# Kernel tuning notes

Hardware: AMD Instinct MI355X
Metric: run time of the kernel (lower is better)

Reference implementation:

```python
import jax, jax.numpy as jnp
import numpy as np
from math import factorial

N_NODES = 20000
N_EDGES = 80000
NUM_GRAPHS = 64
NUM_NEIGHBORS = 3.8
POOL_NODES = 4.0  # num_nodes=4 constant in source forward

# ---------------- real Wigner 3j (e3nn-style, Frobenius norm 1) ----------------

def _w3j_complex(j1, j2, j3, m1, m2, m3):
    if m1 + m2 + m3 != 0:
        return 0.0
    t1 = j2 - m1 - j3; t2 = j1 + m2 - j3; t3 = j1 + j2 - j3
    t4 = j1 - m1; t5 = j2 + m2
    tmin = max(0, t1, t2); tmax = min(t3, t4, t5)
    if tmin > tmax:
        return 0.0
    s = 0.0
    for t in range(tmin, tmax + 1):
        s += (-1.0) ** t / (factorial(t) * factorial(t - t1) * factorial(t - t2)
                            * factorial(t3 - t) * factorial(t4 - t) * factorial(t5 - t))
    tri = (factorial(j1 + j2 - j3) * factorial(j1 - j2 + j3) * factorial(-j1 + j2 + j3)
           / factorial(j1 + j2 + j3 + 1))
    norm = np.sqrt(tri * factorial(j1 + m1) * factorial(j1 - m1) * factorial(j2 + m2)
                   * factorial(j2 - m2) * factorial(j3 + m3) * factorial(j3 - m3))
    return (-1.0) ** (j1 - j2 - m3) * norm * s


def _real_basis(l):
    U = np.zeros((2 * l + 1, 2 * l + 1), dtype=np.complex128)
    U[l, l] = 1.0
    for m in range(1, l + 1):
        U[l + m, l + m] = (-1) ** m / np.sqrt(2.0)
        U[l + m, l - m] = 1.0 / np.sqrt(2.0)
        U[l - m, l - m] = 1j / np.sqrt(2.0)
        U[l - m, l + m] = -1j * (-1) ** m / np.sqrt(2.0)
    return U

_W3J_CACHE = {}

def w3j(l1, l2, l3):
    key = (l1, l2, l3)
    if key not in _W3J_CACHE:
        C = np.zeros((2 * l1 + 1, 2 * l2 + 1, 2 * l3 + 1), dtype=np.complex128)
        for m1 in range(-l1, l1 + 1):
            for m2 in range(-l2, l2 + 1):
                m3 = -(m1 + m2)
                if -l3 <= m3 <= l3:
                    C[m1 + l1, m2 + l2, m3 + l3] = _w3j_complex(l1, l2, l3, m1, m2, m3)
        C = np.einsum('ia,jb,kc,abc->ijk', _real_basis(l1), _real_basis(l2), _real_basis(l3), C)
        C = np.real((-1j) ** (l1 + l2 + l3) * C)
        _W3J_CACHE[key] = jnp.asarray(C, dtype=jnp.float32)
    return _W3J_CACHE[key]

# ---------------- irreps bookkeeping ----------------
SH        = [(1, 0, 1), (1, 1, -1), (1, 2, 1), (1, 3, -1)]            # 1x0e+1x1o+1x2e+1x3o (dim 16)
GATE1_IN  = [(16,0,1),(16,0,-1),(8,0,1),(8,0,-1),(8,0,1),(8,0,-1),(16,1,-1),(16,1,1)]  # dim 160
GATE1_OUT = [(16,0,1),(16,0,1),(16,1,-1),(16,1,1)]                     # dim 128
GATE2_IN  = [(16,0,1),(16,0,-1),(6,0,1),(6,0,-1),(6,0,1),(6,0,-1),(12,1,-1),(12,1,1)]  # dim 128
GATE2_OUT = [(16,0,1),(16,0,1),(12,1,-1),(12,1,1)]                     # dim 104
OUT_FINAL = [(1, 0, 1)]


def slices(irreps):
    out = []; o = 0
    for m, l, p in irreps:
        d = m * (2 * l + 1); out.append((o, o + d)); o += d
    return out


def tp_paths(ir1, ir2, iro):
    paths = []
    for i1, (m1, l1, p1) in enumerate(ir1):
        for i2, (m2, l2, p2) in enumerate(ir2):
            for io, (mo, lo, po) in enumerate(iro):
                if po == p1 * p2 and abs(l1 - l2) <= lo <= l1 + l2:
                    paths.append((i1, i2, io))
    fan = [0] * len(iro)
    for i1, i2, io in paths:
        fan[io] += ir1[i1][0] * ir2[i2][0]
    numel = sum(ir1[i1][0] * ir2[i2][0] * iro[io][0] for i1, i2, io in paths)
    return paths, fan, numel


def tensor_product(x1, x2, weights, ir1, ir2, iro):
    # FullyConnectedTensorProduct, component norm, element path normalization
    paths, fan, numel = tp_paths(ir1, ir2, iro)
    s1, s2 = slices(ir1), slices(ir2)
    E = x1.shape[0]
    out_parts = [jnp.zeros((E, m * (2 * l + 1)), x1.dtype) for m, l, p in iro]
    wofs = 0
    for i1, i2, io in paths:
        m1, l1, _ = ir1[i1]; m2, l2, _ = ir2[i2]; mo, lo, _ = iro[io]
        n = m1 * m2 * mo
        w = weights[:, wofs:wofs + n].reshape(E, m1, m2, mo); wofs += n
        a = x1[:, s1[i1][0]:s1[i1][1]].reshape(E, m1, 2 * l1 + 1)
        b = x2[:, s2[i2][0]:s2[i2][1]].reshape(E, m2, 2 * l2 + 1)
        C = w3j(l1, l2, lo)
        pw = np.sqrt((2 * lo + 1) / fan[io])
        seg = jnp.einsum('eui,evj,ijk,euvw->ewk', a, b, C, w) * pw
        out_parts[io] = out_parts[io] + seg.reshape(E, mo * (2 * lo + 1))
    return jnp.concatenate(out_parts, axis=1)

# ---------------- activations / gate ----------------
_xs = np.linspace(-8.0, 8.0, 100001)
_pdf = np.exp(-0.5 * _xs ** 2) / np.sqrt(2 * np.pi)
TANH_NORM = float(1.0 / np.sqrt(np.sum(np.tanh(_xs) ** 2 * _pdf) * (_xs[1] - _xs[0])))
SQRT2 = float(np.sqrt(2.0))
ACT = {'relu': lambda t: jnp.maximum(t, 0.0) * SQRT2,
       'abs':  lambda t: jnp.abs(t),
       'tanh': lambda t: jnp.tanh(t) * TANH_NORM}


def gate_fn(x, scalars, gates, gated):
    o = 0; outs = []
    for m, a in scalars:
        outs.append(ACT[a](x[:, o:o + m])); o += m
    gv = []
    for m, a in gates:
        gv.append(ACT[a](x[:, o:o + m])); o += m
    g = jnp.concatenate(gv, axis=-1)
    gi = 0
    for m, l in gated:
        d = 2 * l + 1
        feat = x[:, o:o + m * d].reshape(-1, m, d)
        outs.append((feat * g[:, gi:gi + m, None]).reshape(-1, m * d))
        o += m * d; gi += m
    return jnp.concatenate(outs, axis=-1)

# ---------------- edge features ----------------

def sh_component(v):
    # real spherical harmonics l=0..3, 'component' normalization, unit input
    x, y, z = v[:, 0], v[:, 1], v[:, 2]
    s3, s5, s15 = np.sqrt(3.0), np.sqrt(5.0), np.sqrt(15.0)
    s7, s42, s70, s105 = np.sqrt(7.0), np.sqrt(42.0), np.sqrt(70.0), np.sqrt(105.0)
    Y0 = jnp.ones_like(x)[:, None]
    Y1 = jnp.stack([s3 * y, s3 * z, s3 * x], -1)
    Y2 = jnp.stack([s15 * x * y, s15 * y * z, 0.5 * s5 * (3 * z * z - 1.0),
                    s15 * x * z, 0.5 * s15 * (x * x - y * y)], -1)
    Y3 = jnp.stack([0.25 * s70 * y * (3 * x * x - y * y), s105 * x * y * z,
                    0.25 * s42 * y * (5 * z * z - 1.0), 0.5 * s7 * z * (5 * z * z - 3.0),
                    0.25 * s42 * x * (5 * z * z - 1.0), 0.5 * s105 * z * (x * x - y * y),
                    0.25 * s70 * x * (x * x - 3 * y * y)], -1)
    return jnp.concatenate([Y0, Y1, Y2, Y3], -1)  # [E,16]


def soft_one_hot(r):
    # soft_one_hot_linspace(start=0.5,end=2.5,number=3,basis='smooth_finite',cutoff=True)
    values = np.linspace(0.5, 2.5, 5)[1:-1]
    step = values[1] - values[0]
    diff = (r[:, None] - values) / step
    def f(u):
        return jnp.where(u > 0, jnp.exp(-1.0 / jnp.where(u > 0, u, 1.0)), 0.0)
    y = 1.14136 * np.exp(2.0) * f(diff + 1.0) * f(1.0 - diff)
    return y * np.sqrt(3.0)


def fc(x, w1, w2):
    # e3nn FullyConnectedNet([3,256,numel], relu)
    h = jnp.maximum(x @ (w1 / np.sqrt(w1.shape[0])), 0.0) * SQRT2
    return h @ (w2 / np.sqrt(w2.shape[0]))


def convolution(node_feats, edge_src, edge_dst, edge_attr, edge_scalars, w1, w2, ir_in, ir_out, n_nodes):
    weight = fc(edge_scalars, w1, w2)                                   # [E, numel]
    ef = tensor_product(node_feats[edge_src], edge_attr, weight, ir_in, SH, ir_out)
    return jax.ops.segment_sum(ef, edge_dst, num_segments=n_nodes) / np.sqrt(NUM_NEIGHBORS)


def _forward(pos, w1_1, w2_1, w1_2, w2_2, w1_3, w2_3, edge_src, edge_dst, batch):
    N = pos.shape[0]
    vec = pos[edge_src] - pos[edge_dst]
    r = jnp.sqrt(jnp.sum(vec * vec, axis=1) + 1e-12)
    unit = vec / r[:, None]
    edge_attr = sh_component(unit)
    edge_scalars = soft_one_hot(r)
    x = jax.ops.segment_sum(edge_attr, edge_dst, num_segments=N) / np.sqrt(NUM_NEIGHBORS)
    x = convolution(x, edge_src, edge_dst, edge_attr, edge_scalars, w1_1, w2_1, SH, GATE1_IN, N)
    x = gate_fn(x, [(16, 'relu'), (16, 'abs')], [(8, 'relu'), (8, 'tanh'), (8, 'relu'), (8, 'tanh')], [(16, 1), (16, 1)])
    x = convolution(x, edge_src, edge_dst, edge_attr, edge_scalars, w1_2, w2_2, GATE1_OUT, GATE2_IN, N)
    x = gate_fn(x, [(16, 'relu'), (16, 'abs')], [(6, 'relu'), (6, 'tanh'), (6, 'relu'), (6, 'tanh')], [(12, 1), (12, 1)])
    x = convolution(x, edge_src, edge_dst, edge_attr, edge_scalars, w1_3, w2_3, GATE2_OUT, OUT_FINAL, N)
    x = jax.ops.segment_sum(x, batch, num_segments=NUM_GRAPHS) / np.sqrt(POOL_NODES)
    return jax.nn.sigmoid(x)


def setup_inputs():
    key = jax.random.key(0)
    ks = jax.random.split(key, 10)
    pos = jax.random.normal(ks[0], (N_NODES, 3), jnp.float32) * 1.5
    edge_src = jax.random.randint(ks[1], (N_EDGES,), 0, N_NODES)
    edge_dst = jax.random.randint(ks[2], (N_EDGES,), 0, N_NODES)
    batch = jnp.sort(jax.random.randint(ks[3], (N_NODES,), 0, NUM_GRAPHS))
    _, _, n1 = tp_paths(SH, SH, GATE1_IN)
    _, _, n2 = tp_paths(GATE1_OUT, SH, GATE2_IN)
    _, _, n3 = tp_paths(GATE2_OUT, SH, OUT_FINAL)
    w1_1 = jax.random.normal(ks[4], (3, 256), jnp.float32)
    w2_1 = jax.random.normal(ks[5], (256, n1), jnp.float32)
    w1_2 = jax.random.normal(ks[6], (3, 256), jnp.float32)
    w2_2 = jax.random.normal(ks[7], (256, n2), jnp.float32)
    w1_3 = jax.random.normal(ks[8], (3, 256), jnp.float32)
    w2_3 = jax.random.normal(ks[9], (256, n3), jnp.float32)
    return {'pos': pos, 'w1_1': w1_1, 'w2_1': w2_1, 'w1_2': w1_2, 'w2_2': w2_2,
            'w1_3': w1_3, 'w2_3': w2_3, 'edge_src': edge_src, 'edge_dst': edge_dst, 'batch': batch}


def reference(pos, w1_1, w2_1, w1_2, w2_2, w1_3, w2_3, edge_src, edge_dst, batch):
    return _forward(pos, w1_1, w2_1, w1_2, w2_2, w1_3, w2_3, edge_src, edge_dst, batch)
```

## Files before the change

kernel.cpp:

```cpp
#include <hip/hip_runtime.h>
#include <math.h>

#define NNODE 20000
#define NEDGE 80000
#define NGRAPH 64

#define OFF_TANH  656
#define OFF_CNT   660
#define OFF_GSUM  664
#define OFF_HIST  7680
#define OFF_OFFS  9728
#define OFF_CUR   11784
#define OFF_EATTR 14336
#define OFF_RBUF  1294336
#define OFF_EINFO 1374336
#define OFF_X0    1694336
#define OFF_Y1    2014336
#define OFF_Y2    5214336
#define OFF_X1    7774336
#define OFF_X2    10334336
#define OFF_TAB   12414336

#define T000 0
#define T110 1
#define T220 10
#define T330 35
#define T011 84
#define T101 93
#define T111 102
#define T121 129
#define T211 174
#define T231 219
#define T321 324
#define T221 429
#define T331 504

#define INV_SQRT_NEIGH 0.5129891760425771f
#define SQRT2F 1.4142135623730951f

struct TabD { int l1,l2,l3,off; };
constexpr TabD HTABS[13] = {
  {0,0,0,T000},{1,1,0,T110},{2,2,0,T220},{3,3,0,T330},
  {0,1,1,T011},{1,0,1,T101},{1,1,1,T111},{1,2,1,T121},
  {2,1,1,T211},{2,3,1,T231},{3,2,1,T321},{2,2,1,T221},{3,3,1,T331}
};

struct CoreD { short a_off, b_off; short l1,l2,l3; short tab; short coff; short m1; };
struct PathD { short core; short wofs, wend, ooff; short mo, lo; float pw; };

constexpr CoreD HCORES1[13] = {
  {0,0, 0,0,0, T000, 0, 1},
  {0,1, 0,1,1, T011, 1, 1},
  {1,0, 1,0,1, T101, 4, 1},
  {1,1, 1,1,0, T110, 7, 1},
  {1,1, 1,1,1, T111, 8, 1},
  {1,4, 1,2,1, T121, 11, 1},
  {4,1, 2,1,1, T211, 14, 1},
  {4,4, 2,2,0, T220, 17, 1},
  {4,4, 2,2,1, T221, 18, 1},
  {4,9, 2,3,1, T231, 21, 1},
  {9,4, 3,2,1, T321, 24, 1},
  {9,9, 3,3,0, T330, 27, 1},
  {9,9, 3,3,1, T331, 28, 1}
};
#define PWR 0.7071067811865476f
constexpr PathD HPATHS1[21] = {
  {0,  0, 16,  0,16,0,0.5f},
  {0, 16, 24, 32, 8,0,0.5f},
  {0, 24, 32, 48, 8,0,0.5f},
  {1, 32, 48, 64,16,1,PWR},
  {2, 48, 64, 64,16,1,PWR},
  {3, 64, 80,  0,16,0,0.5f},
  {3, 80, 88, 32, 8,0,0.5f},
  {3, 88, 96, 48, 8,0,0.5f},
  {4, 96,112,112,16,1,1.0f},
  {5,112,128, 64,16,1,PWR},
  {6,128,144, 64,16,1,PWR},
  {7,144,160,  0,16,0,0.5f},
  {7,160,168, 32, 8,0,0.5f},
  {7,168,176, 48, 8,0,0.5f},
  {8,176,192,112,16,1,1.0f},
  {9,192,208, 64,16,1,PWR},
  {10,208,224,64,16,1,PWR},
  {11,224,240, 0,16,0,0.5f},
  {11,240,248,32, 8,0,0.5f},
  {11,248,256,48, 8,0,0.5f},
  {12,256,272,112,16,1,1.0f}
};

constexpr CoreD HCORES2[12] = {
  {0,0,  0,0,0, T000, 0,   16},
  {0,1,  0,1,1, T011, 16,  16},
  {16,0, 0,0,0, T000, 64,  16},
  {16,1, 0,1,1, T011, 80,  16},
  {32,0, 1,0,1, T101, 128, 16},
  {32,1, 1,1,0, T110, 176, 16},
  {32,1, 1,1,1, T111, 192, 16},
  {32,4, 1,2,1, T121, 240, 16},
  {80,0, 1,0,1, T101, 288, 16},
  {80,1, 1,1,0, T110, 336, 16},
  {80,1, 1,1,1, T111, 352, 16},
  {80,4, 1,2,1, T121, 400, 16}
};
#define PA 0.14433756729740643f
#define PB 0.25f
#define PC 0.19364916731037085f
constexpr PathD HPATHS2[20] = {
  {0,   0, 256,  0,16,0,PA},
  {0, 256, 352, 32, 6,0,PA},
  {0, 352, 448, 44, 6,0,PA},
  {1, 448, 640, 56,12,1,PC},
  {2, 640, 896,  0,16,0,PA},
  {2, 896, 992, 32, 6,0,PA},
  {2, 992,1088, 44, 6,0,PA},
  {3,1088,1280, 56,12,1,PC},
  {4,1280,1472, 56,12,1,PC},
  {5,1472,1728,  0,16,0,PA},
  {5,1728,1824, 32, 6,0,PA},
  {5,1824,1920, 44, 6,0,PA},
  {6,1920,2112, 92,12,1,PB},
  {7,2112,2304, 56,12,1,PC},
  {8,2304,2496, 92,12,1,PB},
  {9,2496,2752, 16,16,0,PB},
  {9,2752,2848, 38, 6,0,PB},
  {9,2848,2944, 50, 6,0,PB},
  {10,2944,3136,56,12,1,PC},
  {11,3136,3328,92,12,1,PB}
};

constexpr CoreD HCORES3[3] = {
  {0,0,  0,0,0, T000, 0,  16},
  {16,0, 0,0,0, T000, 16, 16},
  {32,1, 1,1,0, T110, 32, 12}
};
#define PD 0.15075567228888181f
constexpr PathD HPATHS3[3] = {
  {0, 0,16, 0,1,0,PD},
  {1,16,32, 0,1,0,PD},
  {2,32,44, 0,1,0,PD}
};

constexpr double FACT[9] = {1.0,1.0,2.0,6.0,24.0,120.0,720.0,5040.0,40320.0};

constexpr double csqrt_(double x){
  if(x<=0.0) return 0.0;
  double g = (x<1.0)? 1.0 : x;
  for(int i=0;i<40;i++) g = 0.5*(g + x/g);
  return g;
}

constexpr double cw3j_(int j1,int j2,int j3,int m1,int m2,int m3){
  if(m1+m2+m3!=0) return 0.0;
  int t1=j2-m1-j3, t2=j1+m2-j3, t3=j1+j2-j3, t4=j1-m1, t5=j2+m2;
  int tmin=t1>0?t1:0; if(t2>tmin) tmin=t2;
  int tmax=t3<t4?t3:t4; if(t5<tmax) tmax=t5;
  if(tmin>tmax) return 0.0;
  double s=0.0;
  for(int t=tmin;t<=tmax;++t){
    double d=FACT[t]*FACT[t-t1]*FACT[t-t2]*FACT[t3-t]*FACT[t4-t]*FACT[t5-t];
    s += ((t&1)? -1.0:1.0)/d;
  }
  double tri=FACT[j1+j2-j3]*FACT[j1-j2+j3]*FACT[-j1+j2+j3]/FACT[j1+j2+j3+1];
  double nrm=csqrt_(tri*FACT[j1+m1]*FACT[j1-m1]*FACT[j2+m2]*FACT[j2-m2]*FACT[j3+m3]*FACT[j3-m3]);
  return (((j1-j2-m3)&1)? -1.0:1.0)*nrm*s;
}

constexpr int curow_(int l,int i,int* a,double* re,double* im){
  const double is2=0.7071067811865475;
  int m=i-l;
  if(m==0){ a[0]=l; re[0]=1.0; im[0]=0.0; return 1; }
  if(m>0){
    a[0]=l+m; re[0]=((m&1)? -is2:is2); im[0]=0.0;
    a[1]=l-m; re[1]=is2; im[1]=0.0; return 2;
  }
  int mm=-m;
  a[0]=l-mm; re[0]=0.0; im[0]=is2;
  a[1]=l+mm; re[1]=0.0; im[1]=((mm&1)? is2:-is2);
  return 2;
}

constexpr float cw3j_elem_(int l1,int l2,int l3,int i,int j,int k){
  int aa[2]={0,0},bb[2]={0,0},cc[2]={0,0};
  double ar[2]={0,0},ai[2]={0,0},br[2]={0,0},bi[2]={0,0},cr[2]={0,0},ci[2]={0,0};
  int na=curow_(l1,i,aa,ar,ai);
  int nb=curow_(l2,j,bb,br,bi);
  int nc=curow_(l3,k,cc,cr,ci);
  double accr=0.0, acci=0.0;
  for(int x=0;x<na;x++)for(int y=0;y<nb;y++)for(int w=0;w<nc;w++){
    double wv=cw3j_(l1,l2,l3, aa[x]-l1, bb[y]-l2, cc[w]-l3);
    if(wv==0.0) continue;
    double pr=ar[x]*br[y]-ai[x]*bi[y];
    double pi=ar[x]*bi[y]+ai[x]*br[y];
    double qr=pr*cr[w]-pi*ci[w];
    double qi=pr*ci[w]+pi*cr[w];
    accr+=qr*wv; acci+=qi*wv;
  }
  int Lm=(l1+l2+l3)&3;
  double res = (Lm==0)? accr : (Lm==1)? acci : (Lm==2)? -accr : -acci;
  return (float)res;
}

struct WApart { float v[429]; };
constexpr WApart gen_wa_(){
  WApart o{};
  for(int t=0;t<11;t++){
    int l1=HTABS[t].l1,l2=HTABS[t].l2,l3=HTABS[t].l3;
    int n2=2*l2+1,n3=2*l3+1;
    int tot=(2*l1+1)*n2*n3;
    for(int z=0;z<tot;z++){
      int i=z/(n2*n3), j=(z/n3)%n2, k=z%n3;
      o.v[HTABS[t].off+z]=cw3j_elem_(l1,l2,l3,i,j,k);
    }
  }
  return o;
}
struct WBpart { float v[222]; };
constexpr WBpart gen_wb_(){
  WBpart o{};
  for(int t=11;t<13;t++){
    int l1=HTABS[t].l1,l2=HTABS[t].l2,l3=HTABS[t].l3;
    int n2=2*l2+1,n3=2*l3+1;
    int tot=(2*l1+1)*n2*n3;
    for(int z=0;z<tot;z++){
      int i=z/(n2*n3), j=(z/n3)%n2, k=z%n3;
      o.v[HTABS[t].off-429+z]=cw3j_elem_(l1,l2,l3,i,j,k);
    }
  }
  return o;
}
constexpr WApart WAC = gen_wa_();
constexpr WBpart WBC = gen_wb_();
struct W3Full { float v[651]; };
constexpr W3Full gen_wfull_(){
  W3Full f{};
  for(int i=0;i<429;i++) f.v[i]=WAC.v[i];
  for(int i=0;i<222;i++) f.v[429+i]=WBC.v[i];
  return f;
}
__constant__ W3Full W3JC = gen_wfull_();

template<int NW> struct PwArr { float v[NW]; };
template<int NW,int NP>
constexpr PwArr<NW> gen_pw_(const PathD (&P)[NP]){
  PwArr<NW> a{};
  for(int p=0;p<NP;p++)
    for(int j=P[p].wofs;j<P[p].wend;j++) a.v[j]=P[p].pw;
  return a;
}
__constant__ PwArr<272>  PWC1 = gen_pw_<272>(HPATHS1);
__constant__ PwArr<3328> PWC2 = gen_pw_<3328>(HPATHS2);
__constant__ PwArr<44>   PWC3 = gen_pw_<44>(HPATHS3);

struct OutSeg { int mult, l; };
constexpr OutSeg OSEG1[8] = {{16,0},{16,0},{8,0},{8,0},{8,0},{8,0},{16,1},{16,1}};
constexpr OutSeg OSEG2[8] = {{16,0},{16,0},{6,0},{6,0},{6,0},{6,0},{12,1},{12,1}};
constexpr OutSeg OSEG3[1] = {{1,0}};

struct Ent2 { int jb, cb, nu; };
template<int NCOL,int NENT,int NW> struct ColMetaT {
  int cidx[NCOL+1];
  int obase[NCOL];
  int n3c[NCOL];
  Ent2 ent[NENT];
  int newj[NW];
};

template<int NCOL,int NENT,int NW,int NSEG,int NP,int NC>
constexpr ColMetaT<NCOL,NENT,NW> gen_colmeta_(const OutSeg (&S)[NSEG], const PathD (&P)[NP], const CoreD (&C)[NC]){
  ColMetaT<NCOL,NENT,NW> m{};
  int col=0, cnt=0, o=0, nb=0;
  for(int s=0;s<NSEG;s++){
    int n3=2*S[s].l+1;
    for(int wc=0;wc<S[s].mult;wc++){
      m.cidx[col]=cnt;
      int ob=o+wc*n3;
      m.obase[col]=ob;
      m.n3c[col]=n3;
      for(int p=0;p<NP;p++){
        PathD pd=P[p];
        int pn3=2*pd.lo+1;
        if(pn3!=n3) continue;
        int rel=ob-pd.ooff;
        if(rel<0||rel>=pd.mo*pn3) continue;
        int w=rel/pn3;
        CoreD cd=C[pd.core];
        int m1=cd.m1;
        m.ent[cnt]=Ent2{nb,(int)cd.coff,m1};
        for(int u=0;u<m1;u++) m.newj[pd.wofs + w + u*pd.mo]=nb+u;
        nb+=m1;
        cnt++;
      }
      col++;
    }
    o+=S[s].mult*n3;
  }
  m.cidx[col]=cnt;
  return m;
}

__constant__ ColMetaT<96,272,272>  CMETA1 = gen_colmeta_<96,272,272>(OSEG1, HPATHS1, HCORES1);
__constant__ ColMetaT<80,208,3328> CMETA2 = gen_colmeta_<80,208,3328>(OSEG2, HPATHS2, HCORES2);
__constant__ ColMetaT< 1,  3,  44> CMETA3 = gen_colmeta_< 1,  3,  44>(OSEG3, HPATHS3, HCORES3);

struct CItem { short aoff, boff, n1, n2, cofs, jstep, woff, pad; };
struct CArr1 { CItem it[31]; };
constexpr CArr1 gen_c1_(){
  CArr1 a{}; int s=0;
  for(int cn=0;cn<13;cn++){
    CoreD cd=HCORES1[cn];
    int n1=2*cd.l1+1,n2=2*cd.l2+1,n3=2*cd.l3+1;
    for(int k=0;k<n3;k++){
      a.it[s]=CItem{cd.a_off,cd.b_off,(short)n1,(short)n2,(short)(cd.tab+k),(short)n3,(short)(cd.coff+k),0};
      s++;
    }
  }
  return a;
}
__constant__ CArr1 CIT1 = gen_c1_();

struct Fam { short b_off, tab, n1, n2, n3, goff; };
constexpr Fam GF2[6]={
  {0,T000,1,1,1,0},{1,T011,1,3,3,1},{0,T101,3,1,3,4},
  {1,T110,3,3,1,13},{1,T111,3,3,3,16},{4,T121,3,5,3,25}};
constexpr Fam GF3[2]={{0,T000,1,1,1,0},{1,T110,3,3,1,1}};
struct CoreG { short fam,a_off,m1,coff; };
constexpr CoreG CG2[12]={
  {0,0,16,0},{1,0,16,16},{0,16,16,64},{1,16,16,80},
  {2,32,16,128},{3,32,16,176},{4,32,16,192},{5,32,16,240},
  {2,80,16,288},{3,80,16,336},{4,80,16,352},{5,80,16,400}};
constexpr CoreG CG3[3]={{0,0,16,0},{0,16,16,16},{1,32,12,32}};

struct GItem { short boff, cofs, n2, jstep; };
template<int NG> struct GArrT { GItem it[NG]; };
template<int NG,int NF>
constexpr GArrT<NG> gen_g_(const Fam (&F)[NF]){
  GArrT<NG> a{}; int s=0;
  for(int f=0;f<NF;f++){
    for(int i=0;i<F[f].n1;i++)for(int k=0;k<F[f].n3;k++){
      a.it[s]=GItem{F[f].b_off,(short)(F[f].tab + i*F[f].n2*F[f].n3 + k),F[f].n2,F[f].n3};
      s++;
    }
  }
  return a;
}
__constant__ GArrT<34> GIT2=gen_g_<34>(GF2);
__constant__ GArrT<4>  GIT3=gen_g_<4>(GF3);

struct OItem { short aoff, gofs, n1, n3, woff, pad; };
template<int NO> struct OArrT { OItem it[NO]; };
template<int NO,int NC,int NF>
constexpr OArrT<NO> gen_o_(const CoreG (&C)[NC], const Fam (&F)[NF]){
  OArrT<NO> a{}; int s=0;
  for(int cn=0;cn<NC;cn++){
    Fam f=F[C[cn].fam];
    for(int k=0;k<f.n3;k++)for(int u=0;u<C[cn].m1;u++){
      a.it[s]=OItem{(short)(C[cn].a_off+u*f.n1),(short)(f.goff+k),f.n1,f.n3,
                    (short)(C[cn].coff+k*C[cn].m1+u),0};
      s++;
    }
  }
  return a;
}
__constant__ OArrT<448> OIT2=gen_o_<448,12,6>(CG2,GF2);
__constant__ OArrT<44>  OIT3=gen_o_<44,3,2>(CG3,GF3);

template<int CNT,int N3,int NCOLS>
__device__ __forceinline__ void apply1_col(const Ent2* __restrict__ ep, const float* __restrict__ T0,
    const float* __restrict__ crb, float fr, float&a0,float&a1,float&a2){
  const float* tja=T0+ep[0].jb;
  float wv[CNT];
  #pragma unroll
  for(int t=0;t<CNT;t++){
    float w0=tja[t], w1=tja[t+NCOLS];
    wv[t]=w0+fr*(w1-w0);
  }
  #pragma unroll
  for(int t=0;t<CNT;t++){
    const float* cr=crb+ep[t].cb;
    a0=fmaf(wv[t],cr[0],a0);
    if constexpr(N3==3){ a1=fmaf(wv[t],cr[1],a1); a2=fmaf(wv[t],cr[2],a2); }
  }
}
__device__ __forceinline__ void apply1_dyn(const Ent2* __restrict__ ep, int cnt, int n3,
    const float* __restrict__ T0, const float* __restrict__ crb, float fr, int NCOLS,
    float&a0,float&a1,float&a2){
  const float* tja=T0+ep[0].jb;
  for(int t=0;t<cnt;t++){
    float w0=tja[t], w1=tja[t+NCOLS];
    float w=w0+fr*(w1-w0);
    const float* cr=crb+ep[t].cb;
    a0=fmaf(w,cr[0],a0);
    if(n3==3){ a1=fmaf(w,cr[1],a1); a2=fmaf(w,cr[2],a2); }
  }
}
template<int CNT,int N3,int NCOLS>
__device__ __forceinline__ void apply2_col(const Ent2* __restrict__ ep, const float* __restrict__ T0,
    const float* __restrict__ crb, float fr, float&a0,float&a1,float&a2){
  #pragma unroll
  for(int t=0;t<CNT;t++){
    const float* cr=crb+ep[t].cb;
    const float* tj=T0+ep[t].jb;
    #pragma unroll
    for(int uu=0;uu<16;uu+=4){
      float4 w0=*(const float4*)(tj+uu);
      float4 w1=*(const float4*)(tj+NCOLS+uu);
      float w;
      if constexpr(N3==1){
        float4 cv=*(const float4*)(cr+uu);
        w=w0.x+fr*(w1.x-w0.x); a0=fmaf(w,cv.x,a0);
        w=w0.y+fr*(w1.y-w0.y); a0=fmaf(w,cv.y,a0);
        w=w0.z+fr*(w1.z-w0.z); a0=fmaf(w,cv.z,a0);
        w=w0.w+fr*(w1.w-w0.w); a0=fmaf(w,cv.w,a0);
      } else {
        float4 c0=*(const float4*)(cr+uu);
        float4 c1=*(const float4*)(cr+16+uu);
        float4 c2=*(const float4*)(cr+32+uu);
        w=w0.x+fr*(w1.x-w0.x); a0=fmaf(w,c0.x,a0); a1=fmaf(w,c1.x,a1); a2=fmaf(w,c2.x,a2);
        w=w0.y+fr*(w1.y-w0.y); a0=fmaf(w,c0.y,a0); a1=fmaf(w,c1.y,a1); a2=fmaf(w,c2.y,a2);
        w=w0.z+fr*(w1.z-w0.z); a0=fmaf(w,c0.z,a0); a1=fmaf(w,c1.z,a1); a2=fmaf(w,c2.z,a2);
        w=w0.w+fr*(w1.w-w0.w); a0=fmaf(w,c0.w,a0); a1=fmaf(w,c1.w,a1); a2=fmaf(w,c2.w,a2);
      }
    }
  }
}
__device__ __forceinline__ void apply2_dyn(const Ent2* __restrict__ ep, int cnt, int n3,
    const float* __restrict__ T0, const float* __restrict__ crb, float fr, int NCOLS,
    float&a0,float&a1,float&a2){
  for(int t=0;t<cnt;t++){
    const float* cr=crb+ep[t].cb;
    const float* tj=T0+ep[t].jb;
    #pragma unroll
    for(int uu=0;uu<16;uu+=4){
      float4 w0=*(const float4*)(tj+uu);
      float4 w1=*(const float4*)(tj+NCOLS+uu);
      float w;
      if(n3==1){
        float4 cv=*(const float4*)(cr+uu);
        w=w0.x+fr*(w1.x-w0.x); a0=fmaf(w,cv.x,a0);
        w=w0.y+fr*(w1.y-w0.y); a0=fmaf(w,cv.y,a0);
        w=w0.z+fr*(w1.z-w0.z); a0=fmaf(w,cv.z,a0);
        w=w0.w+fr*(w1.w-w0.w); a0=fmaf(w,cv.w,a0);
      } else {
        float4 c0=*(const float4*)(cr+uu);
        float4 c1=*(const float4*)(cr+16+uu);
        float4 c2=*(const float4*)(cr+32+uu);
        w=w0.x+fr*(w1.x-w0.x); a0=fmaf(w,c0.x,a0); a1=fmaf(w,c1.x,a1); a2=fmaf(w,c2.x,a2);
        w=w0.y+fr*(w1.y-w0.y); a0=fmaf(w,c0.y,a0); a1=fmaf(w,c1.y,a1); a2=fmaf(w,c2.y,a2);
        w=w0.z+fr*(w1.z-w0.z); a0=fmaf(w,c0.z,a0); a1=fmaf(w,c1.z,a1); a2=fmaf(w,c2.z,a2);
        w=w0.w+fr*(w1.w-w0.w); a0=fmaf(w,c0.w,a0); a1=fmaf(w,c1.w,a1); a2=fmaf(w,c2.w,a2);
      }
    }
  }
}

__global__ __launch_bounds__(256) void k_tables(
    const float* __restrict__ W1_1, const float* __restrict__ W2_1, float* __restrict__ T1,
    const float* __restrict__ W1_2, const float* __restrict__ W2_2, float* __restrict__ T2,
    const float* __restrict__ W1_3, const float* __restrict__ W2_3, float* __restrict__ T3,
    int R, int NR, float* __restrict__ ws){
  int tid=threadIdx.x;
  int by=blockIdx.y;
  if(by==16){
    if(blockIdx.x!=0) return;
    for(int i=tid;i<(728-OFF_CNT);i+=256) ws[OFF_CNT+i]=0.0f;
    for(int i=tid;i<(13832-OFF_HIST);i+=256) ws[OFF_HIST+i]=0.0f;
    __shared__ double red[256];
    double loc=0.0;
    for(int i=tid;i<=100000;i+=256){
      float x=-8.0f+16.0f*(float)i/100000.0f;
      float th=tanhf(x);
      float pdf=expf(-0.5f*x*x)*0.3989422804014327f;
      loc += (double)(th*th*pdf);
    }
    red[tid]=loc; __syncthreads();
    for(int s=128;s>0;s>>=1){ if(tid<s) red[tid]+=red[tid+s]; __syncthreads(); }
    if(tid==0) ws[OFF_TANH]=(float)(1.0/sqrt(red[0]*(16.0/100000.0)));
    return;
  }
  int conv, ybase;
  const float* W1; const float* W2; float* tab; int NCOLS; float scale;
  if(by<2){ conv=1; ybase=by;   W1=W1_1; W2=W2_1; tab=T1; NCOLS=272;  scale=INV_SQRT_NEIGH; }
  else if(by<15){ conv=2; ybase=by-2; W1=W1_2; W2=W2_2; tab=T2; NCOLS=3328; scale=INV_SQRT_NEIGH; }
  else { conv=3; ybase=0;  W1=W1_3; W2=W2_3; tab=T3; NCOLS=44;   scale=INV_SQRT_NEIGH*0.5f; }

  __shared__ float sh_h[256][16];
  int r0=blockIdx.x*16;
  {
    int c=tid;
    float wa=W1[c], wb=W1[256+c], wc=W1[512+c];
    const float A=(float)(1.14136*7.38905609893065*1.7320508075688772);
    for(int k=0;k<16;k++){
      int ri=r0+k;
      float r=0.5f+2.0f*(float)ri/(float)NR;
      float sv[3];
      #pragma unroll
      for(int j=0;j<3;j++){
        float v=1.0f+0.5f*(float)j;
        float diff=(r-v)*2.0f;
        float u1=diff+1.0f, u2=1.0f-diff;
        float f1=(u1>0.0f)? expf(-1.0f/u1):0.0f;
        float f2=(u2>0.0f)? expf(-1.0f/u2):0.0f;
        sv[j]=A*f1*f2;
      }
      float hv=sv[0]*wa+sv[1]*wb+sv[2]*wc;
      hv=fmaxf(hv*0.5773502691896258f,0.0f)*(SQRT2F*0.0625f);
      sh_h[c][k]=hv;
    }
  }
  __syncthreads();
  int j=ybase*256+tid;
  if(j>=NCOLS) return;
  const float* PW=(conv==1)? PWC1.v : (conv==2)? PWC2.v : PWC3.v;
  const int* NJ=(conv==1)? CMETA1.newj : (conv==2)? CMETA2.newj : CMETA3.newj;
  float cs=scale*PW[j];
  int jn=NJ[j];
  float acc[16];
  #pragma unroll
  for(int k=0;k<16;k++) acc[k]=0.0f;
  for(int c=0;c<256;c++){
    float w2v=W2[(size_t)c*NCOLS+j];
    const float4* hp=(const float4*)(&sh_h[c][0]);
    float4 h0=hp[0],h1=hp[1],h2=hp[2],h3=hp[3];
    acc[0]=fmaf(h0.x,w2v,acc[0]);  acc[1]=fmaf(h0.y,w2v,acc[1]);
    acc[2]=fmaf(h0.z,w2v,acc[2]);  acc[3]=fmaf(h0.w,w2v,acc[3]);
    acc[4]=fmaf(h1.x,w2v,acc[4]);  acc[5]=fmaf(h1.y,w2v,acc[5]);
    acc[6]=fmaf(h1.z,w2v,acc[6]);  acc[7]=fmaf(h1.w,w2v,acc[7]);
    acc[8]=fmaf(h2.x,w2v,acc[8]);  acc[9]=fmaf(h2.y,w2v,acc[9]);
    acc[10]=fmaf(h2.z,w2v,acc[10]); acc[11]=fmaf(h2.w,w2v,acc[11]);
    acc[12]=fmaf(h3.x,w2v,acc[12]); acc[13]=fmaf(h3.y,w2v,acc[13]);
    acc[14]=fmaf(h3.z,w2v,acc[14]); acc[15]=fmaf(h3.w,w2v,acc[15]);
  }
  #pragma unroll
  for(int k=0;k<16;k++){
    int ri=r0+k;
    if(ri<R) tab[(size_t)ri*NCOLS+jn]=acc[k]*cs;
  }
}

__global__ void k_edge(const float* __restrict__ pos, const int* __restrict__ esrc,
                       const int* __restrict__ edst, float* __restrict__ ws, int NR){
  int e = blockIdx.x*256 + threadIdx.x;
  if(e>=NEDGE) return;
  float* eattr=ws+OFF_EATTR;
  float* x0=ws+OFF_X0;
  int s=esrc[e], d=edst[e];
  float x=pos[3*s]-pos[3*d], y=pos[3*s+1]-pos[3*d+1], z=pos[3*s+2]-pos[3*d+2];
  float r=sqrtf(x*x+y*y+z*z+1e-12f);
  float iv=1.0f/r; x*=iv; y*=iv; z*=iv;
  const float s3=1.7320508075688772f, s5=2.2360679774997896f, s15=3.872983346207417f;
  const float s7=2.6457513110645907f, s42=6.48074069840786f, s70=8.366600265340756f, s105=10.246950765959598f;
  float Y[16];
  Y[0]=1.0f;
  Y[1]=s3*y; Y[2]=s3*z; Y[3]=s3*x;
  Y[4]=s15*x*y; Y[5]=s15*y*z; Y[6]=0.5f*s5*(3.0f*z*z-1.0f); Y[7]=s15*x*z; Y[8]=0.5f*s15*(x*x-y*y);
  Y[9]=0.25f*s70*y*(3.0f*x*x-y*y); Y[10]=s105*x*y*z; Y[11]=0.25f*s42*y*(5.0f*z*z-1.0f);
  Y[12]=0.5f*s7*z*(5.0f*z*z-3.0f); Y[13]=0.25f*s42*x*(5.0f*z*z-1.0f);
  Y[14]=0.5f*s105*z*(x*x-y*y); Y[15]=0.25f*s70*x*(x*x-3.0f*y*y);
  float4* ep=(float4*)(eattr+(size_t)e*16);
  ep[0]=make_float4(Y[0],Y[1],Y[2],Y[3]);
  ep[1]=make_float4(Y[4],Y[5],Y[6],Y[7]);
  ep[2]=make_float4(Y[8],Y[9],Y[10],Y[11]);
  ep[3]=make_float4(Y[12],Y[13],Y[14],Y[15]);
  #pragma unroll
  for(int i=0;i<16;i++)
    atomicAdd(&x0[(size_t)d*16+i], Y[i]*INV_SQRT_NEIGH);
  ws[OFF_RBUF+e]=r;
  if(r>0.5f && r<2.5f){
    float t=(r-0.5f)*((float)NR*0.5f);
    int i0=min((int)t, NR-1);
    atomicAdd((int*)(ws+OFF_HIST)+i0, 1);
  }
}

__global__ void k_scan(float* __restrict__ ws, int NR){
  __shared__ int sd[2048];
  int t=threadIdx.x;
  int* hist=(int*)(ws+OFF_HIST);
  int* offs=(int*)(ws+OFF_OFFS);
  int i1=t, i2=t+1024;
  sd[i1]=(i1<NR)? hist[i1]:0;
  sd[i2]=(i2<NR)? hist[i2]:0;
  __syncthreads();
  for(int d=1; d<2048; d<<=1){
    int v1=(i1>=d)? sd[i1-d]:0;
    int v2=(i2>=d)? sd[i2-d]:0;
    __syncthreads();
    sd[i1]+=v1; sd[i2]+=v2;
    __syncthreads();
  }
  if(i1<NR) offs[i1]=(i1==0)?0:sd[i1-1];
  if(i2<NR) offs[i2]=sd[i2-1];
  if(t==0){ offs[NR]=sd[NR-1]; *((int*)(ws+OFF_CNT))=sd[NR-1]; }
}

__global__ void k_scatter(const int* __restrict__ esrc, const int* __restrict__ edst,
                          float* __restrict__ ws, int NR){
  int e=blockIdx.x*256+threadIdx.x;
  if(e>=NEDGE) return;
  float r=ws[OFF_RBUF+e];
  if(!(r>0.5f && r<2.5f)) return;
  float t=(r-0.5f)*((float)NR*0.5f);
  int i0=min((int)t, NR-1);
  int* offs=(int*)(ws+OFF_OFFS);
  int* cur=(int*)(ws+OFF_CUR);
  int p=offs[i0]+atomicAdd(&cur[i0],1);
  int4 v; v.x=esrc[e]; v.y=edst[e]; v.z=e; v.w=__float_as_int(t);
  ((int4*)(ws+OFF_EINFO))[p]=v;
}

template<int CONV,int DY,int D_IN,int D_OUT,int CSTRIDE,int NCOL,int NCOLS,bool FINAL>
__global__ __launch_bounds__(256,4) void k_conv(
    const float* __restrict__ xin, const float* __restrict__ TAB,
    float* __restrict__ yout, const int* __restrict__ batchp,
    float* __restrict__ ws, int NR)
{
  constexpr int APAD = D_IN+4;
  constexpr int NGP  = (CONV==2)?36:4;
  constexpr int YST  = (CONV==3)?132:4;
  constexpr int NGV  = (CONV==2)?32:((CONV==3)?24:1);
  __shared__ float sh_a[8][APAD];
  __shared__ float sh_b[8][20];
  __shared__ float sh_core[8][CSTRIDE];
  __shared__ float sh_g[8][NGP];
  __shared__ float sh_gv[8][NGV];
  __shared__ float sh_y[8][YST];
  __shared__ float sh_red[8];
  __shared__ int sh_src[8], sh_dst[8], sh_eid[8];
  __shared__ float sh_t[8];

  int tid=threadIdx.x;
  int nact=*(const int*)(ws+OFF_CNT);
  int base=blockIdx.x*8;
  if(base>=nact) return;
  int ne=min(8, nact-base);

  if(tid<8){
    int src=0,dst=0,eid=-1; float tv=0.0f;
    if(tid<ne){
      int4 v=((const int4*)(ws+OFF_EINFO))[base+tid];
      src=v.x; dst=v.y; eid=v.z; tv=__int_as_float(v.w);
    }
    sh_src[tid]=src; sh_dst[tid]=dst; sh_eid[tid]=eid; sh_t[tid]=tv;
    if constexpr(CONV==3) sh_red[tid]=0.0f;
  }
  __syncthreads();

  if(tid<32){
    int idx=tid>>2, c4=tid&3;
    int eid=sh_eid[idx];
    float4 v=make_float4(0.f,0.f,0.f,0.f);
    if(eid>=0) v=((const float4*)(ws+OFF_EATTR+(size_t)eid*16))[c4];
    *(float4*)&sh_b[idx][c4*4]=v;
  }
  if constexpr(CONV==1){
    if(tid>=32 && tid<64){
      int t2=tid-32; int idx=t2>>2, c4=t2&3;
      float4 v=make_float4(0.f,0.f,0.f,0.f);
      if(sh_eid[idx]>=0) v=((const float4*)(xin+(size_t)sh_src[idx]*16))[c4];
      *(float4*)&sh_a[idx][c4*4]=v;
    }
  } else {
    constexpr int YQ=DY/4;
    for(int z=tid; z<8*YQ; z+=256){
      int idx=z/YQ, c4=z-idx*YQ;
      float4 v=make_float4(0.f,0.f,0.f,0.f);
      if(sh_eid[idx]>=0) v=((const float4*)(xin+(size_t)sh_src[idx]*DY))[c4];
      if constexpr(CONV==2) *(float4*)&sh_core[idx][c4*4]=v;
      else                  *(float4*)&sh_y[idx][c4*4]=v;
    }
  }
  __syncthreads();

  if constexpr(CONV==1){
    constexpr int NIT=31;
    for(int z=tid; z<8*NIT; z+=256){
      int idx=z/NIT, rem=z-idx*NIT;
      CItem it=CIT1.it[rem];
      float acc=0.0f;
      for(int i=0;i<it.n1;i++){
        float av=sh_a[idx][it.aoff+i];
        int cb=it.cofs + i*it.n2*it.jstep;
        for(int j=0;j<it.n2;j++)
          acc += av*sh_b[idx][it.boff+j]*W3JC.v[cb + j*it.jstep];
      }
      sh_core[idx][it.woff]=acc;
    }
    __syncthreads();
  } else {
    float TN=ws[OFF_TANH];
    for(int z=tid; z<8*NGV; z+=256){
      int idx=z/NGV, m=z-idx*NGV;
      const float* yr=(CONV==2)? &sh_core[idx][0] : &sh_y[idx][0];
      float u=yr[32+m];
      bool th=(CONV==2)? (((m>>3)&1)!=0) : (((m/6)&1)!=0);
      sh_gv[idx][m]= th? tanhf(u)*TN : fmaxf(u,0.0f)*SQRT2F;
    }
    constexpr int NG=(CONV==2)?34:4;
    for(int z=tid; z<8*NG; z+=256){
      int idx=z/NG, rem=z-idx*NG;
      GItem it=(CONV==2)? GIT2.it[rem] : GIT3.it[rem];
      float acc=0.0f;
      for(int j=0;j<it.n2;j++)
        acc += sh_b[idx][it.boff+j]*W3JC.v[it.cofs + j*it.jstep];
      sh_g[idx][rem]=acc;
    }
    __syncthreads();
    for(int z=tid; z<8*D_IN; z+=256){
      int idx=z/D_IN, o=z-idx*D_IN;
      const float* yr=(CONV==2)? &sh_core[idx][0] : &sh_y[idx][0];
      float val;
      if(o<16) val=fmaxf(yr[o],0.0f)*SQRT2F;
      else if(o<32) val=fabsf(yr[o]);
      else {
        if constexpr(CONV==2){
          int gi=(o<80)? (o-32)/3 : 16+(o-80)/3;
          val=yr[o+32]*sh_gv[idx][gi];
        } else {
          int gi=(o<68)? (o-32)/3 : 12+(o-68)/3;
          val=yr[o+24]*sh_gv[idx][gi];
        }
      }
      sh_a[idx][o]=val;
    }
    __syncthreads();
    constexpr int NO=(CONV==2)?448:44;
    for(int z=tid; z<8*NO; z+=256){
      int idx=z/NO, rem=z-idx*NO;
      OItem it=(CONV==2)? OIT2.it[rem] : OIT3.it[rem];
      float acc=0.0f;
      #pragma unroll 3
      for(int i=0;i<it.n1;i++)
        acc += sh_a[idx][it.aoff+i]*sh_g[idx][it.gofs + i*it.n3];
      sh_core[idx][it.woff]=acc;
    }
    __syncthreads();
  }

  if constexpr(CONV==3){
    if(tid<88){
      int e3=tid&7, c=tid>>3;
      float tv=sh_t[e3];
      int i0=min((int)tv, NR-1);
      float fr=tv-(float)i0;
      const float* tj=TAB+(size_t)i0*NCOLS + c*4;
      float4 w0=*(const float4*)tj;
      float4 w1=*(const float4*)(tj+NCOLS);
      float4 cv=*(const float4*)(&sh_core[e3][c*4]);
      float p;
      p  = (w0.x+fr*(w1.x-w0.x))*cv.x;
      p += (w0.y+fr*(w1.y-w0.y))*cv.y;
      p += (w0.z+fr*(w1.z-w0.z))*cv.z;
      p += (w0.w+fr*(w1.w-w0.w))*cv.w;
      atomicAdd(&sh_red[e3], p);
    }
    __syncthreads();
    if(tid<ne) atomicAdd(&ws[OFF_GSUM+batchp[sh_dst[tid]]], sh_red[tid]);
  } else {
    int e=tid&7;
    float tv=sh_t[e];
    int i0=min((int)tv, NR-1);
    float fr=tv-(float)i0;
    const float* T0=TAB+(size_t)i0*NCOLS;
    const float* crb=&sh_core[e][0];
    int dstv=sh_dst[e];
    bool act=(e<ne);

    for(int q=tid; q<8*NCOL; q+=256){
      int c=q>>3;
      int s0,s1,ob,n3;
      const Ent2* entp;
      if constexpr(CONV==1){ s0=CMETA1.cidx[c]; s1=CMETA1.cidx[c+1]; ob=CMETA1.obase[c]; n3=CMETA1.n3c[c]; entp=CMETA1.ent; }
      else                 { s0=CMETA2.cidx[c]; s1=CMETA2.cidx[c+1]; ob=CMETA2.obase[c]; n3=CMETA2.n3c[c]; entp=CMETA2.ent; }
      int cnt=s1-s0;
      if(!cnt) continue;
      float a0=0.0f,a1=0.0f,a2=0.0f;
      const Ent2* ep=entp+s0;
      if constexpr(CONV==1){
        if(n3==1){
          switch(cnt){
            case 4: apply1_col<4,1,272>(ep,T0,crb,fr,a0,a1,a2); break;
            default: apply1_dyn(ep,cnt,1,T0,crb,fr,272,a0,a1,a2); break;
          }
        } else {
          switch(cnt){
            case 6: apply1_col<6,3,272>(ep,T0,crb,fr,a0,a1,a2); break;
            case 3: apply1_col<3,3,272>(ep,T0,crb,fr,a0,a1,a2); break;
            default: apply1_dyn(ep,cnt,3,T0,crb,fr,272,a0,a1,a2); break;
          }
        }
      } else {
        if(n3==1){
          switch(cnt){
            case 3: apply2_col<3,1,3328>(ep,T0,crb,fr,a0,a1,a2); break;
            case 1: apply2_col<1,1,3328>(ep,T0,crb,fr,a0,a1,a2); break;
            default: apply2_dyn(ep,cnt,1,T0,crb,fr,3328,a0,a1,a2); break;
          }
        } else {
          switch(cnt){
            case 5: apply2_col<5,3,3328>(ep,T0,crb,fr,a0,a1,a2); break;
            case 3: apply2_col<3,3,3328>(ep,T0,crb,fr,a0,a1,a2); break;
            default: apply2_dyn(ep,cnt,3,T0,crb,fr,3328,a0,a1,a2); break;
          }
        }
      }
      if(act){
        float* yp=&yout[(size_t)dstv*D_OUT+ob];
        atomicAdd(yp, a0);
        if(n3==3){ atomicAdd(yp+1, a1); atomicAdd(yp+2, a2); }
      }
    }
  }
}

__global__ void k_sig(const float* __restrict__ ws, float* __restrict__ out){
  int g=threadIdx.x;
  if(g<NGRAPH){
    float v=ws[OFF_GSUM+g];
    out[g]=1.0f/(1.0f+expf(-v));
  }
}

extern "C" void kernel_launch(void* const* d_in, const int* in_sizes, int n_in,
                              void* d_out, int out_size, void* d_ws, size_t ws_size,
                              hipStream_t stream){
  const float* pos =(const float*)d_in[0];
  const float* w1_1=(const float*)d_in[1];
  const float* w2_1=(const float*)d_in[2];
  const float* w1_2=(const float*)d_in[3];
  const float* w2_2=(const float*)d_in[4];
  const float* w1_3=(const float*)d_in[5];
  const float* w2_3=(const float*)d_in[6];
  const int* esrc=(const int*)d_in[7];
  const int* edst=(const int*)d_in[8];
  const int* batch=(const int*)d_in[9];
  float* ws=(float*)d_ws;
  float* out=(float*)d_out;

  long availRows = ((long)(ws_size/4) - (long)OFF_TAB)/3644L;
  int R = (availRows < 1025L)? (int)availRows : 1025;
  if(R < 9) R = 9;
  int NR = R-1;
  float* TAB1 = ws + OFF_TAB;
  float* TAB2 = TAB1 + (size_t)R*272;
  float* TAB3 = TAB2 + (size_t)R*3328;

  hipMemsetAsync(ws+OFF_X0, 0, (size_t)(OFF_X1-OFF_X0)*sizeof(float), stream);

  k_tables<<<dim3((R+15)/16,17),256,0,stream>>>(
      w1_1,w2_1,TAB1, w1_2,w2_2,TAB2, w1_3,w2_3,TAB3, R,NR, ws);
  k_edge<<<(NEDGE+255)/256,256,0,stream>>>(pos, esrc, edst, ws, NR);
  k_scan<<<1,1024,0,stream>>>(ws, NR);
  k_scatter<<<(NEDGE+255)/256,256,0,stream>>>(esrc, edst, ws, NR);

  k_conv<1, 16, 16,160, 33, 96, 272,false><<<(NEDGE+7)/8,256,0,stream>>>(
      ws+OFF_X0, TAB1, ws+OFF_Y1, batch, ws, NR);

  k_conv<2,160,128,128,452, 80,3328,false><<<(NEDGE+7)/8,256,0,stream>>>(
      ws+OFF_Y1, TAB2, ws+OFF_Y2, batch, ws, NR);

  k_conv<3,128,104,  1, 68,  1, 44,true ><<<(NEDGE+7)/8,256,0,stream>>>(
      ws+OFF_Y2, TAB3, nullptr, batch, ws, NR);

  k_sig<<<1,64,0,stream>>>(ws, out);
}
```

Baseline: 404.4 us.

## Register-tile table GEMM with 8x8 per-thread outputs and vectorized weight loads

```diff
diff --git a/kernel.cpp b/kernel.cpp
--- a/kernel.cpp
+++ b/kernel.cpp
@@ -453,6 +453,42 @@
   }
 }
 
+template<int JT>
+__device__ __forceinline__ void table_gemm(const float* __restrict__ W2, float* __restrict__ tab,
+    int NCOLS, float scale, const float* __restrict__ PW, const int* __restrict__ NJ,
+    int jb, const float (*__restrict__ sh_h)[8], int r0, int R){
+  float acc[8][JT];
+  #pragma unroll
+  for(int k=0;k<8;k++)
+    #pragma unroll
+    for(int u=0;u<JT;u++) acc[k][u]=0.0f;
+  const float* w2p=W2+jb;
+  for(int c=0;c<256;c++){
+    float w[JT];
+    const float* wr=w2p+(size_t)c*NCOLS;
+    *(float4*)&w[0]=*(const float4*)wr;
+    if constexpr(JT==8) *(float4*)&w[4]=*(const float4*)(wr+4);
+    float h[8];
+    *(float4*)&h[0]=*(const float4*)&sh_h[c][0];
+    *(float4*)&h[4]=*(const float4*)&sh_h[c][4];
+    #pragma unroll
+    for(int k=0;k<8;k++)
+      #pragma unroll
+      for(int u=0;u<JT;u++)
+        acc[k][u]=fmaf(h[k],w[u],acc[k][u]);
+  }
+  #pragma unroll
+  for(int u=0;u<JT;u++){
+    float cs=scale*PW[jb+u];
+    int jn=NJ[jb+u];
+    #pragma unroll
+    for(int k=0;k<8;k++){
+      int ri=r0+k;
+      if(ri<R) tab[(size_t)ri*NCOLS+jn]=acc[k][u]*cs;
+    }
+  }
+}
+
 __global__ __launch_bounds__(256) void k_tables(
     const float* __restrict__ W1_1, const float* __restrict__ W2_1, float* __restrict__ T1,
     const float* __restrict__ W1_2, const float* __restrict__ W2_2, float* __restrict__ T2,
@@ -460,7 +496,7 @@
     int R, int NR, float* __restrict__ ws){
   int tid=threadIdx.x;
   int by=blockIdx.y;
-  if(by==16){
+  if(by==4){
     if(blockIdx.x!=0) return;
     for(int i=tid;i<(728-OFF_CNT);i+=256) ws[OFF_CNT+i]=0.0f;
     for(int i=tid;i<(13832-OFF_HIST);i+=256) ws[OFF_HIST+i]=0.0f;
@@ -477,19 +513,20 @@
     if(tid==0) ws[OFF_TANH]=(float)(1.0/sqrt(red[0]*(16.0/100000.0)));
     return;
   }
-  int conv, ybase;
+  int conv, jb0;
   const float* W1; const float* W2; float* tab; int NCOLS; float scale;
-  if(by<2){ conv=1; ybase=by;   W1=W1_1; W2=W2_1; tab=T1; NCOLS=272;  scale=INV_SQRT_NEIGH; }
-  else if(by<15){ conv=2; ybase=by-2; W1=W1_2; W2=W2_2; tab=T2; NCOLS=3328; scale=INV_SQRT_NEIGH; }
-  else { conv=3; ybase=0;  W1=W1_3; W2=W2_3; tab=T3; NCOLS=44;   scale=INV_SQRT_NEIGH*0.5f; }
-
-  __shared__ float sh_h[256][16];
-  int r0=blockIdx.x*16;
+  if(by==0){ conv=1; jb0=0; W1=W1_1; W2=W2_1; tab=T1; NCOLS=272;  scale=INV_SQRT_NEIGH; }
+  else if(by<=2){ conv=2; jb0=(by-1)*2048; W1=W1_2; W2=W2_2; tab=T2; NCOLS=3328; scale=INV_SQRT_NEIGH; }
+  else { conv=3; jb0=0; W1=W1_3; W2=W2_3; tab=T3; NCOLS=44;   scale=INV_SQRT_NEIGH*0.5f; }
+
+  __shared__ float sh_h[256][8];
+  int r0=blockIdx.x*8;
   {
     int c=tid;
     float wa=W1[c], wb=W1[256+c], wc=W1[512+c];
     const float A=(float)(1.14136*7.38905609893065*1.7320508075688772);
-    for(int k=0;k<16;k++){
+    #pragma unroll
+    for(int k=0;k<8;k++){
       int ri=r0+k;
       float r=0.5f+2.0f*(float)ri/(float)NR;
       float sv[3];
@@ -508,32 +545,14 @@
     }
   }
   __syncthreads();
-  int j=ybase*256+tid;
-  if(j>=NCOLS) return;
   const float* PW=(conv==1)? PWC1.v : (conv==2)? PWC2.v : PWC3.v;
   const int* NJ=(conv==1)? CMETA1.newj : (conv==2)? CMETA2.newj : CMETA3.newj;
-  float cs=scale*PW[j];
-  int jn=NJ[j];
-  float acc[16];
-  #pragma unroll
-  for(int k=0;k<16;k++) acc[k]=0.0f;
-  for(int c=0;c<256;c++){
-    float w2v=W2[(size_t)c*NCOLS+j];
-    const float4* hp=(const float4*)(&sh_h[c][0]);
-    float4 h0=hp[0],h1=hp[1],h2=hp[2],h3=hp[3];
-    acc[0]=fmaf(h0.x,w2v,acc[0]);  acc[1]=fmaf(h0.y,w2v,acc[1]);
-    acc[2]=fmaf(h0.z,w2v,acc[2]);  acc[3]=fmaf(h0.w,w2v,acc[3]);
-    acc[4]=fmaf(h1.x,w2v,acc[4]);  acc[5]=fmaf(h1.y,w2v,acc[5]);
-    acc[6]=fmaf(h1.z,w2v,acc[6]);  acc[7]=fmaf(h1.w,w2v,acc[7]);
-    acc[8]=fmaf(h2.x,w2v,acc[8]);  acc[9]=fmaf(h2.y,w2v,acc[9]);
-    acc[10]=fmaf(h2.z,w2v,acc[10]); acc[11]=fmaf(h2.w,w2v,acc[11]);
-    acc[12]=fmaf(h3.x,w2v,acc[12]); acc[13]=fmaf(h3.y,w2v,acc[13]);
-    acc[14]=fmaf(h3.z,w2v,acc[14]); acc[15]=fmaf(h3.w,w2v,acc[15]);
-  }
-  #pragma unroll
-  for(int k=0;k<16;k++){
-    int ri=r0+k;
-    if(ri<R) tab[(size_t)ri*NCOLS+jn]=acc[k]*cs;
+  if(conv==3){
+    int jb=tid*4;
+    if(jb+4<=NCOLS) table_gemm<4>(W2,tab,NCOLS,scale,PW,NJ,jb,sh_h,r0,R);
+  } else {
+    int jb=jb0+tid*8;
+    if(jb+8<=NCOLS) table_gemm<8>(W2,tab,NCOLS,scale,PW,NJ,jb,sh_h,r0,R);
   }
 }
 
@@ -846,7 +865,7 @@
 
   hipMemsetAsync(ws+OFF_X0, 0, (size_t)(OFF_X1-OFF_X0)*sizeof(float), stream);
 
-  k_tables<<<dim3((R+15)/16,17),256,0,stream>>>(
+  k_tables<<<dim3((R+7)/8,5),256,0,stream>>>(
       w1_1,w2_1,TAB1, w1_2,w2_2,TAB2, w1_3,w2_3,TAB3, R,NR, ws);
   k_edge<<<(NEDGE+255)/256,256,0,stream>>>(pos, esrc, edst, ws, NR);
   k_scan<<<1,1024,0,stream>>>(ws, NR);
```

Measured after the change: 383.2 us. 5.2% less time.
